# Kernel optimization log

Hardware: AMD Instinct MI355X
Metric: run time of the kernel (lower is better)

## Reference

```python
import jax, jax.numpy as jnp
from jax import lax
import numpy as np

VOCAB = 100000
MAX_SEQ = 8192
DIM = 128
K = 5
STRIDE = 1
PAD = 2


def setup_inputs() -> dict:
    key = jax.random.key(0)
    ks = jax.random.split(key, 6)
    X = jax.random.randint(ks[0], (8, 8192), 0, VOCAB, dtype=jnp.int64)
    # nn.Linear(vocab, dim): weight (dim, vocab), bias (dim)
    W_lin = jax.random.normal(ks[1], (DIM, VOCAB), dtype=jnp.float32) * 0.02
    b_lin = jax.random.normal(ks[2], (DIM,), dtype=jnp.float32) * 0.02
    # nn.Conv1d(dim, dim, k): weight (out=dim, in=dim, k), bias (dim)
    W_conv = jax.random.normal(ks[3], (DIM, DIM, K), dtype=jnp.float32) * 0.02
    b_conv = jax.random.normal(ks[4], (DIM,), dtype=jnp.float32) * 0.02
    # nn.Embedding(max_seq_len, dim)
    pos_table = jax.random.normal(ks[5], (MAX_SEQ, DIM), dtype=jnp.float32) * 0.02
    return {"X": X, "W_lin": W_lin, "b_lin": b_lin,
            "W_conv": W_conv, "b_conv": b_conv, "pos_table": pos_table}


def reference(X, W_lin, b_lin, W_conv, b_conv, pos_table):
    # one_hot(X) @ W_lin.T + b_lin  ==  gather rows of W_lin.T
    emb = jnp.take(W_lin.T, X, axis=0) + b_lin          # (b, n, d)
    x = jnp.transpose(emb, (0, 2, 1))                   # (b, d, n)
    y = lax.conv_general_dilated(
        x, W_conv, window_strides=(STRIDE,), padding=[(PAD, PAD)],
        dimension_numbers=("NCH", "OIH", "NCH"))
    y = y + b_conv[None, :, None]                       # (b, d, n_out)
    tokens = jnp.transpose(y, (0, 2, 1))                # (b, n_out, d)
    n_out = tokens.shape[1]
    return tokens + pos_table[:n_out][None, :, :]
```

## Files before the change

### kernel.cpp

```cpp
#include <hip/hip_runtime.h>
#include <hip/hip_bf16.h>
#include <stdint.h>

#define VOCAB 100000
#define SEQ   8192
#define BATCH 8
#define DIM   128

#define WLT_BLOCKS 1563
#define WCONV_BLOCKS 320

typedef short bf16x8 __attribute__((ext_vector_type(8)));
typedef float f32x4  __attribute__((ext_vector_type(4)));

__device__ __forceinline__ ushort f2bf(float f) {
  union { float f; uint32_t u; } v; v.f = f;
  uint32_t u = v.u;
  return (ushort)((u + 0x7FFF + ((u >> 16) & 1)) >> 16);
}

__global__ __launch_bounds__(256) void prep(
    const float* __restrict__ wlin, const float* __restrict__ blin,
    const float* __restrict__ wconv, ushort* __restrict__ wlt,
    ushort* __restrict__ wcb) {
  __shared__ float tile[128 * 65];
  const int tid = threadIdx.x;

  if (blockIdx.x >= WLT_BLOCKS) {
    int e = (blockIdx.x - WLT_BLOCKS) * 256 + tid;
    int k = e / (DIM * DIM);
    int rem = e % (DIM * DIM);
    int d = rem / DIM, i = rem % DIM;
    wcb[e] = f2bf(wconv[(d * DIM + i) * 5 + k]);
    return;
  }

  const int t0 = blockIdx.x * 64;

  const int c4 = (tid & 15) * 4;
  const int rbase = tid >> 4;
  const bool cvalid = (t0 + c4) < VOCAB;
#pragma unroll
  for (int p = 0; p < 8; ++p) {
    int r = p * 16 + rbase;
    float4 v = make_float4(0.f, 0.f, 0.f, 0.f);
    if (cvalid) v = *(const float4*)(wlin + (size_t)r * VOCAB + t0 + c4);
    float* dst = &tile[r * 65 + c4];
    dst[0] = v.x; dst[1] = v.y; dst[2] = v.z; dst[3] = v.w;
  }
  __syncthreads();

  const int chunk = tid & 15;
  float bias8[8];
#pragma unroll
  for (int j = 0; j < 8; ++j) bias8[j] = blin[chunk * 8 + j];

#pragma unroll
  for (int p = 0; p < 4; ++p) {
    int tl = (tid >> 4) + p * 16;
    int t  = t0 + tl;
    if (t >= VOCAB) continue;
    ushort u[8];
#pragma unroll
    for (int j = 0; j < 8; ++j)
      u[j] = f2bf(tile[(chunk * 8 + j) * 65 + tl] + bias8[j]);
    *(uint4*)(wlt + (size_t)t * DIM + chunk * 8) = *(const uint4*)u;
  }
}

template <bool EDGE>
__device__ __forceinline__ void conv_wave(
    const int* __restrict__ Xb, const ushort* __restrict__ wlt,
    const ushort* __restrict__ wcb, const float* __restrict__ bconv,
    const float* __restrict__ pos, float* __restrict__ outb,
    int n0, int lr, int lq) {
  int  tok[2][5];
  bool vld[2][5];
#pragma unroll
  for (int mt = 0; mt < 2; ++mt)
#pragma unroll
    for (int k = 0; k < 5; ++k) {
      int n = n0 + mt * 16 + lr + k - 2;
      bool v = EDGE ? (n >= 0 && n < SEQ) : true;
      vld[mt][k] = v;
      tok[mt][k] = v ? Xb[n] : 0;
    }

  f32x4 acc[2][8];
#pragma unroll
  for (int mt = 0; mt < 2; ++mt)
#pragma unroll
    for (int nt = 0; nt < 8; ++nt) acc[mt][nt] = (f32x4)0.f;

  const int colA = lq * 8;
#pragma unroll
  for (int k = 0; k < 5; ++k) {
    bf16x8 A[2][4];
#pragma unroll
    for (int mt = 0; mt < 2; ++mt)
#pragma unroll
      for (int kk = 0; kk < 4; ++kk) {
        bf16x8 v = *(const bf16x8*)(wlt + ((size_t)tok[mt][k] << 7) + kk * 32 + colA);
        A[mt][kk] = (EDGE && !vld[mt][k]) ? (bf16x8)(short)0 : v;
      }
#pragma unroll
    for (int kk = 0; kk < 4; ++kk) {
      bf16x8 B[8];
#pragma unroll
      for (int nt = 0; nt < 8; ++nt)
        B[nt] = *(const bf16x8*)(wcb +
            ((size_t)(k * DIM + nt * 16 + lr) * DIM + kk * 32 + colA));
#pragma unroll
      for (int mt = 0; mt < 2; ++mt)
#pragma unroll
        for (int nt = 0; nt < 8; ++nt)
          acc[mt][nt] = __builtin_amdgcn_mfma_f32_16x16x32_bf16(
              A[mt][kk], B[nt], acc[mt][nt], 0, 0, 0);
    }
  }

  float bc[8];
#pragma unroll
  for (int nt = 0; nt < 8; ++nt) bc[nt] = bconv[nt * 16 + lr];
#pragma unroll
  for (int mt = 0; mt < 2; ++mt) {
#pragma unroll
    for (int rr = 0; rr < 4; ++rr) {
      int gn = n0 + mt * 16 + lq * 4 + rr;
      const float* posrow = pos + (size_t)gn * DIM;
      float* orow = outb + (size_t)gn * DIM;
#pragma unroll
      for (int nt = 0; nt < 8; ++nt) {
        int d = nt * 16 + lr;
        orow[d] = acc[mt][nt][rr] + bc[nt] + posrow[d];
      }
    }
  }
}

__global__ __launch_bounds__(256, 2) void conv_main(
    const int* __restrict__ X, const ushort* __restrict__ wlt,
    const ushort* __restrict__ wcb, const float* __restrict__ bconv,
    const float* __restrict__ pos, float* __restrict__ out) {
  const int tid  = threadIdx.x;
  const int wave = tid >> 6;
  const int lane = tid & 63;
  const int lr   = lane & 15;
  const int lq   = lane >> 4;
  const int gw    = blockIdx.x * 4 + wave;
  const int batch = gw >> 8;
  const int n0    = (gw & 255) << 5;
  const int* Xb   = X + batch * SEQ;
  float* outb     = out + (size_t)batch * SEQ * DIM;

  if (n0 == 0 || n0 == SEQ - 32)
    conv_wave<true>(Xb, wlt, wcb, bconv, pos, outb, n0, lr, lq);
  else
    conv_wave<false>(Xb, wlt, wcb, bconv, pos, outb, n0, lr, lq);
}

extern "C" void kernel_launch(void* const* d_in, const int* in_sizes, int n_in,
                              void* d_out, int out_size, void* d_ws, size_t ws_size,
                              hipStream_t stream) {
  const int*   X     = (const int*)d_in[0];
  const float* wlin  = (const float*)d_in[1];
  const float* blin  = (const float*)d_in[2];
  const float* wconv = (const float*)d_in[3];
  const float* bconv = (const float*)d_in[4];
  const float* pos   = (const float*)d_in[5];
  float*       out   = (float*)d_out;

  ushort* wcb = (ushort*)d_ws;
  ushort* wlt = (ushort*)((char*)d_ws + 262144);

  hipLaunchKernelGGL(prep, dim3(WLT_BLOCKS + WCONV_BLOCKS), dim3(256), 0, stream,
                     wlin, blin, wconv, wlt, wcb);
  hipLaunchKernelGGL(conv_main, dim3(512), dim3(256), 0, stream,
                     X, wlt, wcb, bconv, pos, out);
}
```

Measured before the change: 161.3 us.

## Split conv output channels across blocks and stage conv weights in LDS

Each block now covers 128 positions and one quarter (32) of the output channels, so the grid grows from 512 to 2048 blocks. Each block copies its 40 KB slice of bf16 conv weights into shared memory in MFMA fragment order, and waves then read B operands from LDS instead of global memory. This is meant to raise parallelism and occupancy (launch bounds now target 4 blocks) and cut register pressure from 16 to 4 accumulators per wave. In exchange, every embedding row (A operand) is gathered four times, once per channel quarter, and each block pays a weight preload plus a barrier.

After: 160.5 us. About the same (-0.5%).

```diff
diff --git a/kernel.cpp b/kernel.cpp
--- a/kernel.cpp
+++ b/kernel.cpp
@@ -71,9 +71,9 @@
 template <bool EDGE>
 __device__ __forceinline__ void conv_wave(
     const int* __restrict__ Xb, const ushort* __restrict__ wlt,
-    const ushort* __restrict__ wcb, const float* __restrict__ bconv,
+    const ushort* __restrict__ Blds, const float* __restrict__ bconv,
     const float* __restrict__ pos, float* __restrict__ outb,
-    int n0, int lr, int lq) {
+    int n0, int q, int lane, int lr, int lq) {
   int  tok[2][5];
   bool vld[2][5];
 #pragma unroll
@@ -86,11 +86,11 @@
       tok[mt][k] = v ? Xb[n] : 0;
     }
 
-  f32x4 acc[2][8];
+  f32x4 acc[2][2];
 #pragma unroll
-  for (int mt = 0; mt < 2; ++mt)
+  for (int a = 0; a < 2; ++a)
 #pragma unroll
-    for (int nt = 0; nt < 8; ++nt) acc[mt][nt] = (f32x4)0.f;
+    for (int b = 0; b < 2; ++b) acc[a][b] = (f32x4)0.f;
 
   const int colA = lq * 8;
 #pragma unroll
@@ -105,23 +105,22 @@
       }
 #pragma unroll
     for (int kk = 0; kk < 4; ++kk) {
-      bf16x8 B[8];
+      bf16x8 B[2];
 #pragma unroll
-      for (int nt = 0; nt < 8; ++nt)
-        B[nt] = *(const bf16x8*)(wcb +
-            ((size_t)(k * DIM + nt * 16 + lr) * DIM + kk * 32 + colA));
+      for (int nt = 0; nt < 2; ++nt)
+        B[nt] = *(const bf16x8*)(Blds + (((k * 4 + kk) * 2 + nt) << 9) + lane * 8);
 #pragma unroll
       for (int mt = 0; mt < 2; ++mt)
 #pragma unroll
-        for (int nt = 0; nt < 8; ++nt)
+        for (int nt = 0; nt < 2; ++nt)
           acc[mt][nt] = __builtin_amdgcn_mfma_f32_16x16x32_bf16(
               A[mt][kk], B[nt], acc[mt][nt], 0, 0, 0);
     }
   }
 
-  float bc[8];
+  float bc[2];
 #pragma unroll
-  for (int nt = 0; nt < 8; ++nt) bc[nt] = bconv[nt * 16 + lr];
+  for (int nt = 0; nt < 2; ++nt) bc[nt] = bconv[q * 32 + nt * 16 + lr];
 #pragma unroll
   for (int mt = 0; mt < 2; ++mt) {
 #pragma unroll
@@ -130,33 +129,50 @@
       const float* posrow = pos + (size_t)gn * DIM;
       float* orow = outb + (size_t)gn * DIM;
 #pragma unroll
-      for (int nt = 0; nt < 8; ++nt) {
-        int d = nt * 16 + lr;
+      for (int nt = 0; nt < 2; ++nt) {
+        int d = q * 32 + nt * 16 + lr;
         orow[d] = acc[mt][nt][rr] + bc[nt] + posrow[d];
       }
     }
   }
 }
 
-__global__ __launch_bounds__(256, 2) void conv_main(
+__global__ __launch_bounds__(256, 4) void conv_main(
     const int* __restrict__ X, const ushort* __restrict__ wlt,
     const ushort* __restrict__ wcb, const float* __restrict__ bconv,
     const float* __restrict__ pos, float* __restrict__ out) {
-  const int tid  = threadIdx.x;
+  __shared__ __align__(16) ushort Blds[20480];
+
+  const int tid = threadIdx.x;
+  const int q   = blockIdx.x & 3;
+  const int gb  = blockIdx.x >> 2;
+  const int batch = gb >> 6;
+  const int nbb   = (gb & 63) << 7;
+
+#pragma unroll
+  for (int it = 0; it < 10; ++it) {
+    int s  = it * 256 + tid;
+    int f  = s >> 6, l = s & 63;
+    int k  = f >> 3, kk = (f >> 1) & 3, nt = f & 1;
+    int flr = l & 15, flq = l >> 4;
+    int d  = q * 32 + nt * 16 + flr;
+    uint4 v = *(const uint4*)(wcb + ((size_t)(k * DIM + d) * DIM + kk * 32 + flq * 8));
+    *(uint4*)&Blds[s * 8] = v;
+  }
+  __syncthreads();
+
   const int wave = tid >> 6;
   const int lane = tid & 63;
   const int lr   = lane & 15;
   const int lq   = lane >> 4;
-  const int gw    = blockIdx.x * 4 + wave;
-  const int batch = gw >> 8;
-  const int n0    = (gw & 255) << 5;
-  const int* Xb   = X + batch * SEQ;
-  float* outb     = out + (size_t)batch * SEQ * DIM;
+  const int n0   = nbb + wave * 32;
+  const int* Xb  = X + batch * SEQ;
+  float* outb    = out + (size_t)batch * SEQ * DIM;
 
   if (n0 == 0 || n0 == SEQ - 32)
-    conv_wave<true>(Xb, wlt, wcb, bconv, pos, outb, n0, lr, lq);
+    conv_wave<true>(Xb, wlt, Blds, bconv, pos, outb, n0, q, lane, lr, lq);
   else
-    conv_wave<false>(Xb, wlt, wcb, bconv, pos, outb, n0, lr, lq);
+    conv_wave<false>(Xb, wlt, Blds, bconv, pos, outb, n0, q, lane, lr, lq);
 }
 
 extern "C" void kernel_launch(void* const* d_in, const int* in_sizes, int n_in,
@@ -175,6 +191,6 @@
 
   hipLaunchKernelGGL(prep, dim3(WLT_BLOCKS + WCONV_BLOCKS), dim3(256), 0, stream,
                      wlin, blin, wconv, wlt, wcb);
-  hipLaunchKernelGGL(conv_main, dim3(512), dim3(256), 0, stream,
+  hipLaunchKernelGGL(conv_main, dim3(2048), dim3(256), 0, stream,
                      X, wlt, wcb, bconv, pos, out);
 }
```
